# Optimization experiments

Hardware: AMD Instinct MI355X
Metric: run time of the kernel (lower is better)

The kernel has to match this reference:

```python
import jax, jax.numpy as jnp
import numpy as np

N = 100000   # nodes
E = 1600000  # edges (avg degree 16)
F_IN, F_HID, F_OUT = 128, 64, 16


def setup_inputs() -> dict:
    key = jax.random.key(0)
    ks = jax.random.split(key, 8)
    x = jax.random.normal(ks[0], (N, F_IN), jnp.float32)
    edge_index = jax.random.randint(ks[1], (2, E), 0, N, dtype=jnp.int32)
    def glorot(k, fan_in, fan_out):
        return jax.random.normal(k, (fan_in, fan_out), jnp.float32) * (1.0 / np.sqrt(fan_in))
    return {
        "x": x,
        "edge_index": edge_index,
        "W1": glorot(ks[2], F_IN, F_HID), "b1": jnp.zeros((F_HID,), jnp.float32),
        "W2": glorot(ks[3], F_HID, F_HID), "b2": jnp.zeros((F_HID,), jnp.float32),
        "W3": glorot(ks[4], F_HID, F_HID), "b3": jnp.zeros((F_HID,), jnp.float32),
        "W4": glorot(ks[5], F_HID, F_OUT), "b4": jnp.zeros((F_OUT,), jnp.float32),
    }


def _gcn_norm(edge_index, num_nodes):
    # Add self-loops and compute symmetric normalization D^-1/2 (A+I) D^-1/2
    loop = jnp.arange(num_nodes, dtype=edge_index.dtype)
    src = jnp.concatenate([edge_index[0], loop])
    dst = jnp.concatenate([edge_index[1], loop])
    deg = jax.ops.segment_sum(jnp.ones_like(dst, jnp.float32), dst, num_segments=num_nodes)
    dinv = jnp.where(deg > 0, jax.lax.rsqrt(deg), 0.0)
    norm = dinv[src] * dinv[dst]  # [E+N]
    return src, dst, norm


def _gcn_conv(x, W, b, src, dst, norm, num_nodes):
    h = x @ W                       # [N, F_out] small GEMM first (PyG order)
    msg = h[src] * norm[:, None]    # [E+N, F_out] gather + scale
    out = jax.ops.segment_sum(msg, dst, num_segments=num_nodes)
    return out + b


def reference(x, edge_index, W1, b1, W2, b2, W3, b3, W4, b4):
    src, dst, norm = _gcn_norm(edge_index, N)
    h = jax.nn.relu(_gcn_conv(x, W1, b1, src, dst, norm, N))  # dropout is identity in eval
    h = jax.nn.relu(_gcn_conv(h, W2, b2, src, dst, norm, N))
    h = jax.nn.relu(_gcn_conv(h, W3, b3, src, dst, norm, N))
    return _gcn_conv(h, W4, b4, src, dst, norm, N)
```

## Files before the change

kernel.cpp:

```cpp
#include <hip/hip_runtime.h>
#include <hip/hip_bf16.h>
#include <stdint.h>


#define TPB 256
#define MAXDEG 64
#define NGRP 8

typedef unsigned int uint;
typedef _Float16 h8 __attribute__((ext_vector_type(8)));
typedef _Float16 h16 __attribute__((ext_vector_type(16)));
typedef float f4 __attribute__((ext_vector_type(4)));

__device__ __forceinline__ int swz(int f) {
    return ((f >> 3) & 3) * 16 + (f >> 5) * 8 + (f & 7);
}

__global__ __launch_bounds__(TPB) void k_scatter(const int* __restrict__ src,
                                                 const int* __restrict__ dst,
                                                 uint* __restrict__ cnt,
                                                 int* __restrict__ bucket,
                                                 int E, int chunk) {
    int grp = blockIdx.x & (NGRP - 1);
    int bin = blockIdx.x >> 3;
    int bpg = gridDim.x >> 3;
    int lo = grp * chunk;
    int hi = lo + chunk;
    int tid = bin * TPB + (int)threadIdx.x;
    int tstride = bpg * TPB;
    int nq = E >> 2;
    const int4* dst4 = (const int4*)dst;
    const int4* src4 = (const int4*)src;
    for (int q = tid; q < nq; q += tstride) {
        int4 d = dst4[q];
        bool m0 = (d.x >= lo) & (d.x < hi);
        bool m1 = (d.y >= lo) & (d.y < hi);
        bool m2 = (d.z >= lo) & (d.z < hi);
        bool m3 = (d.w >= lo) & (d.w < hi);
        if (m0 | m1 | m2 | m3) {
            int4 s = src4[q];
            uint p0 = m0 ? atomicAdd(&cnt[d.x], 1u) : 0u;
            uint p1 = m1 ? atomicAdd(&cnt[d.y], 1u) : 0u;
            uint p2 = m2 ? atomicAdd(&cnt[d.z], 1u) : 0u;
            uint p3 = m3 ? atomicAdd(&cnt[d.w], 1u) : 0u;
            if (m0 && p0 < MAXDEG) bucket[(size_t)d.x * MAXDEG + (int)p0] = s.x;
            if (m1 && p1 < MAXDEG) bucket[(size_t)d.y * MAXDEG + (int)p1] = s.y;
            if (m2 && p2 < MAXDEG) bucket[(size_t)d.z * MAXDEG + (int)p2] = s.z;
            if (m3 && p3 < MAXDEG) bucket[(size_t)d.w * MAXDEG + (int)p3] = s.w;
        }
    }
    for (int e = (nq << 2) + tid; e < E; e += tstride) {
        int d = dst[e];
        if (d >= lo && d < hi) {
            uint p = atomicAdd(&cnt[d], 1u);
            if (p < MAXDEG) bucket[(size_t)d * MAXDEG + (int)p] = src[e];
        }
    }
}

__global__ __launch_bounds__(TPB) void k_gemm_mfma128(const float* __restrict__ X,
                                                      const float* __restrict__ W,
                                                      const uint* __restrict__ cnt,
                                                      _Float16* __restrict__ H,
                                                      int ngrp16, int nwaves, int n) {
    const int lane = threadIdx.x & 63;
    const int wid = blockIdx.x * (TPB / 64) + (threadIdx.x >> 6);
    const int nrow = lane & 15;
    const int kgrp = lane >> 4;

    h8 Bf[4][4];
#pragma unroll
    for (int kb = 0; kb < 4; ++kb)
#pragma unroll
        for (int j = 0; j < 8; ++j) {
            int k = kb * 32 + kgrp * 8 + j;
#pragma unroll
            for (int cb = 0; cb < 4; ++cb)
                Bf[kb][cb][j] = (_Float16)W[k * 64 + cb * 16 + nrow];
        }

    for (int g = wid; g < ngrp16; g += nwaves) {
        const int base = g * 16;
        int arow = base + nrow; if (arow >= n) arow = n - 1;
        const float* xr = X + (size_t)arow * 128;
        h8 A[4];
#pragma unroll
        for (int kb = 0; kb < 4; ++kb) {
            f4 lo = *(const f4*)(xr + kb * 32 + kgrp * 8);
            f4 hi = *(const f4*)(xr + kb * 32 + kgrp * 8 + 4);
#pragma unroll
            for (int j = 0; j < 4; ++j) { A[kb][j] = (_Float16)lo[j]; A[kb][4 + j] = (_Float16)hi[j]; }
        }
        f4 D[4];
#pragma unroll
        for (int cb = 0; cb < 4; ++cb) {
            f4 d = {0.f, 0.f, 0.f, 0.f};
#pragma unroll
            for (int kb = 0; kb < 4; ++kb)
                d = __builtin_amdgcn_mfma_f32_16x16x32_f16(A[kb], Bf[kb][cb], d, 0, 0, 0);
            D[cb] = d;
        }
#pragma unroll
        for (int r = 0; r < 4; ++r) {
            int onode = base + kgrp * 4 + r;
            if (onode < n) {
                float dio = rsqrtf((float)cnt[onode] + 1.0f);
#pragma unroll
                for (int cb = 0; cb < 4; ++cb)
                    H[(size_t)onode * 64 + swz(cb * 16 + nrow)] = (_Float16)(D[cb][r] * dio);
            }
        }
    }
}

template <int FOUT>
__global__ __launch_bounds__(TPB, 2) void k_agg_mfma(const _Float16* __restrict__ H,
                                                     const int* __restrict__ bucket,
                                                     const uint* __restrict__ cnt,
                                                     const float* __restrict__ b,
                                                     const float* __restrict__ W,
                                                     _Float16* __restrict__ Hout,
                                                     int ngrp16, int nwaves) {
    const int lane = threadIdx.x & 63;
    const int wid = blockIdx.x * (TPB / 64) + (threadIdx.x >> 6);
    const int nrow = lane & 15;
    const int kgrp = lane >> 4;
    const int kofs = kgrp * 16;
    constexpr int NCB = FOUT / 16;

    h8 Bf[2][NCB];
    float bias[16];
#pragma unroll
    for (int kb = 0; kb < 2; ++kb)
#pragma unroll
        for (int j = 0; j < 8; ++j) {
            int f = kb * 32 + kgrp * 8 + j;
            bias[kb * 8 + j] = b[f];
#pragma unroll
            for (int cb = 0; cb < NCB; ++cb)
                Bf[kb][cb][j] = (_Float16)W[f * FOUT + cb * 16 + nrow];
        }

    for (int g = wid; g < ngrp16; g += nwaves) {
        const int base = g * 16;
        const int node = base + nrow;
        const int cc = (int)cnt[node];
        const int cn = (cc < MAXDEG) ? cc : MAXDEG;

        float acc[16];
        {
            h16 sv = *(const h16*)(H + (size_t)node * 64 + kofs);
#pragma unroll
            for (int j = 0; j < 16; ++j) acc[j] = (float)sv[j];
        }
        const int* eb = bucket + (size_t)node * MAXDEG;
        int t = 0;
        for (; t + 4 <= cn; t += 4) {
            int i0 = eb[t], i1 = eb[t + 1], i2 = eb[t + 2], i3 = eb[t + 3];
            h16 v0 = *(const h16*)(H + (size_t)i0 * 64 + kofs);
            h16 v1 = *(const h16*)(H + (size_t)i1 * 64 + kofs);
            h16 v2 = *(const h16*)(H + (size_t)i2 * 64 + kofs);
            h16 v3 = *(const h16*)(H + (size_t)i3 * 64 + kofs);
#pragma unroll
            for (int j = 0; j < 16; ++j)
                acc[j] += ((float)v0[j] + (float)v1[j]) + ((float)v2[j] + (float)v3[j]);
        }
        if (t + 2 <= cn) {
            int i0 = eb[t], i1 = eb[t + 1];
            h16 v0 = *(const h16*)(H + (size_t)i0 * 64 + kofs);
            h16 v1 = *(const h16*)(H + (size_t)i1 * 64 + kofs);
#pragma unroll
            for (int j = 0; j < 16; ++j) acc[j] += (float)v0[j] + (float)v1[j];
            t += 2;
        }
        if (t < cn) {
            h16 v0 = *(const h16*)(H + (size_t)eb[t] * 64 + kofs);
#pragma unroll
            for (int j = 0; j < 16; ++j) acc[j] += (float)v0[j];
        }

        float di = rsqrtf((float)cc + 1.0f);
        h8 A0, A1;
#pragma unroll
        for (int j = 0; j < 8; ++j) {
            A0[j] = (_Float16)fmaxf(fmaf(di, acc[j], bias[j]), 0.f);
            A1[j] = (_Float16)fmaxf(fmaf(di, acc[8 + j], bias[8 + j]), 0.f);
        }

        f4 D[NCB];
#pragma unroll
        for (int cb = 0; cb < NCB; ++cb) {
            f4 d = {0.f, 0.f, 0.f, 0.f};
            d = __builtin_amdgcn_mfma_f32_16x16x32_f16(A0, Bf[0][cb], d, 0, 0, 0);
            d = __builtin_amdgcn_mfma_f32_16x16x32_f16(A1, Bf[1][cb], d, 0, 0, 0);
            D[cb] = d;
        }
#pragma unroll
        for (int r = 0; r < 4; ++r) {
            int onode = base + kgrp * 4 + r;
            float dio = rsqrtf((float)cnt[onode] + 1.0f);
#pragma unroll
            for (int cb = 0; cb < NCB; ++cb) {
                int f = cb * 16 + nrow;
                int p = (FOUT == 64) ? swz(f) : f;
                Hout[(size_t)onode * FOUT + p] = (_Float16)(D[cb][r] * dio);
            }
        }
    }
}

__global__ __launch_bounds__(TPB) void k_agg16(const _Float16* __restrict__ H,
                                               const int* __restrict__ bucket,
                                               const uint* __restrict__ cnt,
                                               const float* __restrict__ b,
                                               float* __restrict__ Out, int n) {
    int tid = blockIdx.x * TPB + threadIdx.x;
    int node = tid >> 4;
    int feat = tid & 15;
    if (node >= n) return;
    float s0 = (float)H[(size_t)node * 16 + feat];
    float s1 = 0.f, s2 = 0.f, s3 = 0.f, s4 = 0.f, s5 = 0.f, s6 = 0.f, s7 = 0.f;
    const int craw = (int)cnt[node];
    const int cn = (craw < MAXDEG) ? craw : MAXDEG;
    const int* eb = bucket + (size_t)node * MAXDEG;
    int t = 0;
    for (; t + 8 <= cn; t += 8) {
        int i0 = eb[t],     i1 = eb[t + 1], i2 = eb[t + 2], i3 = eb[t + 3];
        int i4 = eb[t + 4], i5 = eb[t + 5], i6 = eb[t + 6], i7 = eb[t + 7];
        float v0 = (float)H[(size_t)i0 * 16 + feat];
        float v1 = (float)H[(size_t)i1 * 16 + feat];
        float v2 = (float)H[(size_t)i2 * 16 + feat];
        float v3 = (float)H[(size_t)i3 * 16 + feat];
        float v4 = (float)H[(size_t)i4 * 16 + feat];
        float v5 = (float)H[(size_t)i5 * 16 + feat];
        float v6 = (float)H[(size_t)i6 * 16 + feat];
        float v7 = (float)H[(size_t)i7 * 16 + feat];
        s0 += v0; s1 += v1; s2 += v2; s3 += v3;
        s4 += v4; s5 += v5; s6 += v6; s7 += v7;
    }
    if (t + 4 <= cn) {
        int i0 = eb[t], i1 = eb[t + 1], i2 = eb[t + 2], i3 = eb[t + 3];
        s0 += (float)H[(size_t)i0 * 16 + feat];
        s1 += (float)H[(size_t)i1 * 16 + feat];
        s2 += (float)H[(size_t)i2 * 16 + feat];
        s3 += (float)H[(size_t)i3 * 16 + feat];
        t += 4;
    }
    if (t + 2 <= cn) {
        int i0 = eb[t], i1 = eb[t + 1];
        s0 += (float)H[(size_t)i0 * 16 + feat];
        s1 += (float)H[(size_t)i1 * 16 + feat];
        t += 2;
    }
    if (t < cn) s0 += (float)H[(size_t)eb[t] * 16 + feat];
    float di = rsqrtf((float)craw + 1.0f);
    float s = ((s0 + s1) + (s2 + s3)) + ((s4 + s5) + (s6 + s7));
    Out[(size_t)node * 16 + feat] = di * s + b[feat];
}

static inline size_t align256(size_t x) { return (x + 255) & ~(size_t)255; }

extern "C" void kernel_launch(void* const* d_in, const int* in_sizes, int n_in,
                              void* d_out, int out_size, void* d_ws, size_t ws_size,
                              hipStream_t stream) {
    const float* x  = (const float*)d_in[0];
    const int* ei   = (const int*)d_in[1];
    const float* W1 = (const float*)d_in[2];
    const float* b1 = (const float*)d_in[3];
    const float* W2 = (const float*)d_in[4];
    const float* b2 = (const float*)d_in[5];
    const float* W3 = (const float*)d_in[6];
    const float* b3 = (const float*)d_in[7];
    const float* W4 = (const float*)d_in[8];
    const float* b4 = (const float*)d_in[9];
    float* out = (float*)d_out;

    const int N = in_sizes[0] / 128;
    const int E = in_sizes[1] / 2;
    const int* src = ei;
    const int* dst = ei + E;

    char* p = (char*)d_ws;
    size_t off = 0;
    uint* cnt = (uint*)(p + off); off += align256((size_t)N * 4);
    size_t zero_bytes = off;
    int* bucket = (int*)(p + off); off += align256((size_t)N * MAXDEG * 4);
    _Float16* hA = (_Float16*)(p + off); off += align256((size_t)N * 64 * 2);
    _Float16* hB = (_Float16*)(p + off); off += align256((size_t)N * 64 * 2);
    (void)ws_size;

    hipMemsetAsync(d_ws, 0, zero_bytes, stream);

    const int chunk = (N + NGRP - 1) / NGRP;
    k_scatter<<<2048, TPB, 0, stream>>>(src, dst, cnt, bucket, E, chunk);

    const int ngrp16 = (N + 15) / 16;
    const int NBLK_M = (ngrp16 + (TPB / 64) - 1) / (TPB / 64);
    const int NWAVES_M = NBLK_M * (TPB / 64);

    k_gemm_mfma128<<<NBLK_M, TPB, 0, stream>>>(x, W1, cnt, hA, ngrp16, NWAVES_M, N);
    k_agg_mfma<64><<<NBLK_M, TPB, 0, stream>>>(hA, bucket, cnt, b1, W2, hB, ngrp16, NWAVES_M);
    k_agg_mfma<64><<<NBLK_M, TPB, 0, stream>>>(hB, bucket, cnt, b2, W3, hA, ngrp16, NWAVES_M);
    k_agg_mfma<16><<<NBLK_M, TPB, 0, stream>>>(hA, bucket, cnt, b3, W4, hB, ngrp16, NWAVES_M);
    int gAgg16 = (N * 16 + TPB - 1) / TPB;
    k_agg16<<<gAgg16, TPB, 0, stream>>>(hB, bucket, cnt, b4, out, N);
}
```

Measured before the change: 239.8 us.

## Replace 8-pass filtered edge scatter with two-phase partition-then-fill bucketing

Before, each of the 8 block groups read the whole dst array and kept only edges landing in its node range, so the edge list was read 8 times. Now one pass partitions edges into 8 per-group FIFOs, using wave ballots and a single atomic per group per wave, with packed (local dst << 17 | src) words. A second kernel then fills the per-node buckets from each group's FIFO, which keeps the node-level atomics localized. This adds a FIFO buffer and an extra launch. The packing assumes src < 2^17 and local dst < 2^15, and edges beyond a group's capacity are dropped.

```diff
diff --git a/kernel.cpp b/kernel.cpp
--- a/kernel.cpp
+++ b/kernel.cpp
@@ -16,45 +16,103 @@
     return ((f >> 3) & 3) * 16 + (f >> 5) * 8 + (f & 7);
 }
 
-__global__ __launch_bounds__(TPB) void k_scatter(const int* __restrict__ src,
-                                                 const int* __restrict__ dst,
-                                                 uint* __restrict__ cnt,
-                                                 int* __restrict__ bucket,
-                                                 int E, int chunk) {
+__device__ __forceinline__ int grp_of(int d, int chunk, float invchunk) {
+    int g = (int)((float)d * invchunk);
+    if (d >= (g + 1) * chunk) ++g;
+    else if (d < g * chunk) --g;
+    return g;
+}
+
+__global__ __launch_bounds__(TPB) void k_part(const int* __restrict__ src,
+                                              const int* __restrict__ dst,
+                                              uint* __restrict__ gctr,
+                                              uint* __restrict__ fifo,
+                                              int E, int chunk, float invchunk, int cap) {
+    int tid = blockIdx.x * TPB + (int)threadIdx.x;
+    int lane = threadIdx.x & 63;
+    int tstride = gridDim.x * TPB;
+    int nq = E >> 2;
+    const int4* dst4 = (const int4*)dst;
+    const int4* src4 = (const int4*)src;
+    unsigned long long lmlt = (lane == 0) ? 0ull : ((~0ull) >> (64 - lane));
+    for (int q = tid; q < nq; q += tstride) {
+        int4 d = dst4[q];
+        int4 s = src4[q];
+        int dd[4] = {d.x, d.y, d.z, d.w};
+        int ss[4] = {s.x, s.y, s.z, s.w};
+        int gg[4];
+#pragma unroll
+        for (int u = 0; u < 4; ++u) gg[u] = grp_of(dd[u], chunk, invchunk);
+        uint pos[4] = {0u, 0u, 0u, 0u};
+#pragma unroll
+        for (int g = 0; g < NGRP; ++g) {
+            unsigned long long m0 = __ballot(gg[0] == g);
+            unsigned long long m1 = __ballot(gg[1] == g);
+            unsigned long long m2 = __ballot(gg[2] == g);
+            unsigned long long m3 = __ballot(gg[3] == g);
+            uint c0 = (uint)__popcll(m0), c1 = (uint)__popcll(m1);
+            uint c2 = (uint)__popcll(m2), c3 = (uint)__popcll(m3);
+            uint total = c0 + c1 + c2 + c3;
+            uint base = 0;
+            if (lane == 0 && total) base = atomicAdd(&gctr[g], total);
+            base = (uint)__shfl((int)base, 0, 64);
+            if (gg[0] == g) pos[0] = base + (uint)__popcll(m0 & lmlt);
+            if (gg[1] == g) pos[1] = base + c0 + (uint)__popcll(m1 & lmlt);
+            if (gg[2] == g) pos[2] = base + c0 + c1 + (uint)__popcll(m2 & lmlt);
+            if (gg[3] == g) pos[3] = base + c0 + c1 + c2 + (uint)__popcll(m3 & lmlt);
+        }
+#pragma unroll
+        for (int u = 0; u < 4; ++u) {
+            int g = gg[u];
+            if (pos[u] < (uint)cap)
+                fifo[(size_t)g * cap + pos[u]] =
+                    ((uint)(dd[u] - g * chunk) << 17) | (uint)ss[u];
+        }
+    }
+    for (int e = (nq << 2) + tid; e < E; e += tstride) {
+        int dv = dst[e], sv = src[e];
+        int g = grp_of(dv, chunk, invchunk);
+        uint p = atomicAdd(&gctr[g], 1u);
+        if (p < (uint)cap)
+            fifo[(size_t)g * cap + p] = ((uint)(dv - g * chunk) << 17) | (uint)sv;
+    }
+}
+
+__global__ __launch_bounds__(TPB) void k_fill(const uint* __restrict__ fifo,
+                                              const uint* __restrict__ gctr,
+                                              uint* __restrict__ cnt,
+                                              int* __restrict__ bucket,
+                                              int chunk, int cap) {
     int grp = blockIdx.x & (NGRP - 1);
     int bin = blockIdx.x >> 3;
     int bpg = gridDim.x >> 3;
-    int lo = grp * chunk;
-    int hi = lo + chunk;
+    int n = (int)gctr[grp];
+    if (n > cap) n = cap;
+    const uint* f = fifo + (size_t)grp * cap;
     int tid = bin * TPB + (int)threadIdx.x;
-    int tstride = bpg * TPB;
-    int nq = E >> 2;
-    const int4* dst4 = (const int4*)dst;
-    const int4* src4 = (const int4*)src;
-    for (int q = tid; q < nq; q += tstride) {
-        int4 d = dst4[q];
-        bool m0 = (d.x >= lo) & (d.x < hi);
-        bool m1 = (d.y >= lo) & (d.y < hi);
-        bool m2 = (d.z >= lo) & (d.z < hi);
-        bool m3 = (d.w >= lo) & (d.w < hi);
-        if (m0 | m1 | m2 | m3) {
-            int4 s = src4[q];
-            uint p0 = m0 ? atomicAdd(&cnt[d.x], 1u) : 0u;
-            uint p1 = m1 ? atomicAdd(&cnt[d.y], 1u) : 0u;
-            uint p2 = m2 ? atomicAdd(&cnt[d.z], 1u) : 0u;
-            uint p3 = m3 ? atomicAdd(&cnt[d.w], 1u) : 0u;
-            if (m0 && p0 < MAXDEG) bucket[(size_t)d.x * MAXDEG + (int)p0] = s.x;
-            if (m1 && p1 < MAXDEG) bucket[(size_t)d.y * MAXDEG + (int)p1] = s.y;
-            if (m2 && p2 < MAXDEG) bucket[(size_t)d.z * MAXDEG + (int)p2] = s.z;
-            if (m3 && p3 < MAXDEG) bucket[(size_t)d.w * MAXDEG + (int)p3] = s.w;
-        }
-    }
-    for (int e = (nq << 2) + tid; e < E; e += tstride) {
-        int d = dst[e];
-        if (d >= lo && d < hi) {
-            uint p = atomicAdd(&cnt[d], 1u);
-            if (p < MAXDEG) bucket[(size_t)d * MAXDEG + (int)p] = src[e];
-        }
+    int tstr = bpg * TPB;
+    int nq = n >> 2;
+    const uint4* f4 = (const uint4*)f;
+    int dbase = grp * chunk;
+    for (int q = tid; q < nq; q += tstr) {
+        uint4 v = f4[q];
+        uint vv[4] = {v.x, v.y, v.z, v.w};
+        int dd[4], ss[4];
+#pragma unroll
+        for (int u = 0; u < 4; ++u) { dd[u] = dbase + (int)(vv[u] >> 17); ss[u] = (int)(vv[u] & 0x1FFFFu); }
+        uint pp[4];
+#pragma unroll
+        for (int u = 0; u < 4; ++u) pp[u] = atomicAdd(&cnt[dd[u]], 1u);
+#pragma unroll
+        for (int u = 0; u < 4; ++u)
+            if (pp[u] < MAXDEG) bucket[(size_t)dd[u] * MAXDEG + (int)pp[u]] = ss[u];
+    }
+    for (int e = (nq << 2) + tid; e < n; e += tstr) {
+        uint v = f[e];
+        int dv = dbase + (int)(v >> 17);
+        int sv = (int)(v & 0x1FFFFu);
+        uint p = atomicAdd(&cnt[dv], 1u);
+        if (p < MAXDEG) bucket[(size_t)dv * MAXDEG + (int)p] = sv;
     }
 }
 
@@ -280,19 +338,25 @@
     const int* src = ei;
     const int* dst = ei + E;
 
+    const int chunk = (N + NGRP - 1) / NGRP;
+    const float invchunk = 1.0f / (float)chunk;
+    const int cap = E / NGRP + 8192;
+
     char* p = (char*)d_ws;
     size_t off = 0;
     uint* cnt = (uint*)(p + off); off += align256((size_t)N * 4);
+    uint* gctr = (uint*)(p + off); off += 256;
     size_t zero_bytes = off;
     int* bucket = (int*)(p + off); off += align256((size_t)N * MAXDEG * 4);
+    uint* fifo = (uint*)(p + off); off += align256((size_t)NGRP * cap * 4);
     _Float16* hA = (_Float16*)(p + off); off += align256((size_t)N * 64 * 2);
     _Float16* hB = (_Float16*)(p + off); off += align256((size_t)N * 64 * 2);
     (void)ws_size;
 
     hipMemsetAsync(d_ws, 0, zero_bytes, stream);
 
-    const int chunk = (N + NGRP - 1) / NGRP;
-    k_scatter<<<2048, TPB, 0, stream>>>(src, dst, cnt, bucket, E, chunk);
+    k_part<<<1024, TPB, 0, stream>>>(src, dst, gctr, fifo, E, chunk, invchunk, cap);
+    k_fill<<<2048, TPB, 0, stream>>>(fifo, gctr, cnt, bucket, chunk, cap);
 
     const int ngrp16 = (N + 15) / 16;
     const int NBLK_M = (ngrp16 + (TPB / 64) - 1) / (TPB / 64);
```

Result: slower. 813.8 us (+239.4%).

## Replace multi-pass edge scatter with two-phase partition and fill

Applied to the files above, without the earlier changes.

The old scatter kernel had every destination group scan the whole dst array, filtering edges by range. It is replaced by a partition kernel that reads each edge once and writes packed (local dst, src) words into per-block, per-group slabs, with a global overflow buffer for spills. A fill kernel then reads each slab and does the atomic bucket insertion for its group. This cuts the repeated reads of the edge arrays, at the cost of an extra kernel launch and a slab write/read round-trip. The slab memory aliases an activation buffer that is not yet in use at that point.

```diff
diff --git a/kernel.cpp b/kernel.cpp
--- a/kernel.cpp
+++ b/kernel.cpp
@@ -6,6 +6,9 @@
 #define TPB 256
 #define MAXDEG 64
 #define NGRP 8
+#define NBLK_P 256
+#define SLABCAP 1536
+#define OVCAP 65536
 
 typedef unsigned int uint;
 typedef _Float16 h8 __attribute__((ext_vector_type(8)));
@@ -16,44 +19,85 @@
     return ((f >> 3) & 3) * 16 + (f >> 5) * 8 + (f & 7);
 }
 
-__global__ __launch_bounds__(TPB) void k_scatter(const int* __restrict__ src,
-                                                 const int* __restrict__ dst,
-                                                 uint* __restrict__ cnt,
-                                                 int* __restrict__ bucket,
-                                                 int E, int chunk) {
-    int grp = blockIdx.x & (NGRP - 1);
-    int bin = blockIdx.x >> 3;
-    int bpg = gridDim.x >> 3;
-    int lo = grp * chunk;
-    int hi = lo + chunk;
-    int tid = bin * TPB + (int)threadIdx.x;
-    int tstride = bpg * TPB;
-    int nq = E >> 2;
-    const int4* dst4 = (const int4*)dst;
-    const int4* src4 = (const int4*)src;
-    for (int q = tid; q < nq; q += tstride) {
-        int4 d = dst4[q];
-        bool m0 = (d.x >= lo) & (d.x < hi);
-        bool m1 = (d.y >= lo) & (d.y < hi);
-        bool m2 = (d.z >= lo) & (d.z < hi);
-        bool m3 = (d.w >= lo) & (d.w < hi);
-        if (m0 | m1 | m2 | m3) {
-            int4 s = src4[q];
-            uint p0 = m0 ? atomicAdd(&cnt[d.x], 1u) : 0u;
-            uint p1 = m1 ? atomicAdd(&cnt[d.y], 1u) : 0u;
-            uint p2 = m2 ? atomicAdd(&cnt[d.z], 1u) : 0u;
-            uint p3 = m3 ? atomicAdd(&cnt[d.w], 1u) : 0u;
-            if (m0 && p0 < MAXDEG) bucket[(size_t)d.x * MAXDEG + (int)p0] = s.x;
-            if (m1 && p1 < MAXDEG) bucket[(size_t)d.y * MAXDEG + (int)p1] = s.y;
-            if (m2 && p2 < MAXDEG) bucket[(size_t)d.z * MAXDEG + (int)p2] = s.z;
-            if (m3 && p3 < MAXDEG) bucket[(size_t)d.w * MAXDEG + (int)p3] = s.w;
-        }
-    }
-    for (int e = (nq << 2) + tid; e < E; e += tstride) {
+__device__ __forceinline__ int grp_of(int d, int chunk, float invchunk) {
+    int g = (int)((float)d * invchunk);
+    if (d >= (g + 1) * chunk) ++g;
+    else if (d < g * chunk) --g;
+    return g;
+}
+
+__global__ __launch_bounds__(TPB) void k_part(const int* __restrict__ src,
+                                              const int* __restrict__ dst,
+                                              uint* __restrict__ pcount,
+                                              uint* __restrict__ ovcnt,
+                                              int* __restrict__ ovbuf,
+                                              uint* __restrict__ slab,
+                                              int E, int chunk, float invchunk,
+                                              int range) {
+    __shared__ uint lcnt[NGRP];
+    if (threadIdx.x < NGRP) lcnt[threadIdx.x] = 0;
+    __syncthreads();
+    const int e0 = blockIdx.x * range;
+    const int e1 = (e0 + range < E) ? e0 + range : E;
+    for (int e = e0 + (int)threadIdx.x; e < e1; e += TPB) {
         int d = dst[e];
-        if (d >= lo && d < hi) {
-            uint p = atomicAdd(&cnt[d], 1u);
-            if (p < MAXDEG) bucket[(size_t)d * MAXDEG + (int)p] = src[e];
+        int s = src[e];
+        int g = grp_of(d, chunk, invchunk);
+        uint pos = atomicAdd(&lcnt[g], 1u);
+        uint val = ((uint)(d - g * chunk) << 17) | (uint)s;
+        if (pos < SLABCAP) {
+            slab[((size_t)blockIdx.x * NGRP + g) * SLABCAP + pos] = val;
+        } else {
+            uint p = atomicAdd(ovcnt, 1u);
+            if (p < OVCAP) { ovbuf[2 * p] = d; ovbuf[2 * p + 1] = s; }
+        }
+    }
+    __syncthreads();
+    if (threadIdx.x < NGRP) {
+        uint c = lcnt[threadIdx.x];
+        pcount[blockIdx.x * NGRP + threadIdx.x] = (c < SLABCAP) ? c : SLABCAP;
+    }
+}
+
+__global__ __launch_bounds__(TPB) void k_fill(const uint* __restrict__ slab,
+                                              const uint* __restrict__ pcount,
+                                              const uint* __restrict__ ovcnt,
+                                              const int* __restrict__ ovbuf,
+                                              uint* __restrict__ cnt,
+                                              int* __restrict__ bucket,
+                                              int chunk) {
+    const int grp = blockIdx.x & (NGRP - 1);
+    const int blk = blockIdx.x >> 3;
+    const int n = (int)pcount[blk * NGRP + grp];
+    const uint* s = slab + ((size_t)blk * NGRP + grp) * SLABCAP;
+    const int dbase = grp * chunk;
+    int e = (int)threadIdx.x;
+    for (; e + TPB < n; e += 2 * TPB) {
+        uint v0 = s[e];
+        uint v1 = s[e + TPB];
+        int d0 = dbase + (int)(v0 >> 17), s0 = (int)(v0 & 0x1FFFFu);
+        int d1 = dbase + (int)(v1 >> 17), s1 = (int)(v1 & 0x1FFFFu);
+        uint p0 = atomicAdd(&cnt[d0], 1u);
+        uint p1 = atomicAdd(&cnt[d1], 1u);
+        if (p0 < MAXDEG) bucket[(size_t)d0 * MAXDEG + (int)p0] = s0;
+        if (p1 < MAXDEG) bucket[(size_t)d1 * MAXDEG + (int)p1] = s1;
+    }
+    if (e < n) {
+        uint v = s[e];
+        int d = dbase + (int)(v >> 17), sv = (int)(v & 0x1FFFFu);
+        uint p = atomicAdd(&cnt[d], 1u);
+        if (p < MAXDEG) bucket[(size_t)d * MAXDEG + (int)p] = sv;
+    }
+    if (blk == 0) {
+        uint on = *ovcnt;
+        if (on > OVCAP) on = OVCAP;
+        for (uint i = threadIdx.x; i < on; i += TPB) {
+            int d = ovbuf[2 * i];
+            if (d >= dbase && d < dbase + chunk) {
+                int sv = ovbuf[2 * i + 1];
+                uint p = atomicAdd(&cnt[d], 1u);
+                if (p < MAXDEG) bucket[(size_t)d * MAXDEG + (int)p] = sv;
+            }
         }
     }
 }
@@ -280,19 +324,29 @@
     const int* src = ei;
     const int* dst = ei + E;
 
+    const int chunk = (N + NGRP - 1) / NGRP;
+    const float invchunk = 1.0f / (float)chunk;
+    const int range = (E + NBLK_P - 1) / NBLK_P;
+
     char* p = (char*)d_ws;
     size_t off = 0;
     uint* cnt = (uint*)(p + off); off += align256((size_t)N * 4);
+    uint* pcount = (uint*)(p + off); off += align256((size_t)NBLK_P * NGRP * 4);
+    uint* ovcnt = (uint*)(p + off); off += 256;
     size_t zero_bytes = off;
     int* bucket = (int*)(p + off); off += align256((size_t)N * MAXDEG * 4);
+    int* ovbuf = (int*)(p + off); off += align256((size_t)OVCAP * 8);
     _Float16* hA = (_Float16*)(p + off); off += align256((size_t)N * 64 * 2);
     _Float16* hB = (_Float16*)(p + off); off += align256((size_t)N * 64 * 2);
+    uint* slab = (uint*)hB;
     (void)ws_size;
 
     hipMemsetAsync(d_ws, 0, zero_bytes, stream);
 
-    const int chunk = (N + NGRP - 1) / NGRP;
-    k_scatter<<<2048, TPB, 0, stream>>>(src, dst, cnt, bucket, E, chunk);
+    k_part<<<NBLK_P, TPB, 0, stream>>>(src, dst, pcount, ovcnt, ovbuf, slab,
+                                       E, chunk, invchunk, range);
+    k_fill<<<NBLK_P * NGRP, TPB, 0, stream>>>(slab, pcount, ovcnt, ovbuf,
+                                              cnt, bucket, chunk);
 
     const int ngrp16 = (N + 15) / 16;
     const int NBLK_M = (ngrp16 + (TPB / 64) - 1) / (TPB / 64);
```

After: 248.7 us. 1.04x slower.
